# Performance work log

Hardware: AMD Instinct MI355X
Metric: run time of the kernel (lower is better)

## Reference

```python
import jax, jax.numpy as jnp
import numpy as np

B, T, C, HS = 4, 2048, 1024, 64

def setup_inputs() -> dict:
    key = jax.random.key(0)
    k1, k2, k3, k4 = jax.random.split(key, 4)
    # weights stored as [n_embd, head_size] so projection is x @ W
    scale = C ** -0.5
    return {
        "x": jax.random.normal(k1, (B, T, C), dtype=jnp.float32),
        "Wq": jax.random.normal(k2, (C, HS), dtype=jnp.float32) * scale,
        "Wk": jax.random.normal(k3, (C, HS), dtype=jnp.float32) * scale,
        "Wv": jax.random.normal(k4, (C, HS), dtype=jnp.float32) * scale,
    }

def reference(x, Wq, Wk, Wv):
    # single-head causal attention: softmax(QK^T / sqrt(hs)) V, dropout p=0 (eval)
    q = x @ Wq  # [B,T,hs]
    k = x @ Wk
    v = x @ Wv
    hs = k.shape[-1]
    wei = jnp.einsum('bqh,bkh->bqk', q, k) * (hs ** -0.5)  # [B,T,T]
    causal = jnp.tril(jnp.ones((q.shape[1], q.shape[1]), dtype=bool))
    wei = jnp.where(causal[None, :, :], wei, -jnp.inf)
    wei = jax.nn.softmax(wei, axis=-1)
    out = jnp.einsum('bqk,bkh->bqh', wei, v)  # [B,T,hs]
    return out
```

## Files before the change

### kernel.cpp

```cpp
#include <hip/hip_runtime.h>
#include <stdint.h>

#define NB 4
#define NT 2048
#define NC 1024
#define NH 64
#define NM (NB*NT)

typedef unsigned short u16;
typedef unsigned int u32;
typedef __bf16 bf16_t;
typedef float f32x4 __attribute__((ext_vector_type(4)));
typedef bf16_t bf16x8 __attribute__((ext_vector_type(8)));
typedef u16 u16x8 __attribute__((ext_vector_type(8)));
typedef u16 u16x4 __attribute__((ext_vector_type(4)));

__device__ __forceinline__ u16 f2b(float f) {
  return __builtin_bit_cast(u16, (bf16_t)f);
}

__device__ __forceinline__ void gl16(const void* g, void* l) {
  __builtin_amdgcn_global_load_lds(
      (const __attribute__((address_space(1))) u32*)g,
      (__attribute__((address_space(3))) u32*)l, 16, 0, 0);
}

__global__ __launch_bounds__(256) void wt_kernel(const float* __restrict__ Wq,
                                                 const float* __restrict__ Wk,
                                                 const float* __restrict__ Wv,
                                                 u16* __restrict__ wt) {
  __shared__ float t[64][65];
  const int m = blockIdx.x >> 4;
  const int kt = blockIdx.x & 15;
  const int k0 = kt * 64;
  const float* W = (m == 0) ? Wq : (m == 1) ? Wk : Wv;
  {
    const int r = threadIdx.x >> 2, c4 = threadIdx.x & 3;
    #pragma unroll
    for (int j = 0; j < 4; ++j) {
      const float4 f = *(const float4*)(W + (size_t)(k0 + r) * NH + c4 * 16 + j * 4);
      t[r][c4 * 16 + j * 4 + 0] = f.x;
      t[r][c4 * 16 + j * 4 + 1] = f.y;
      t[r][c4 * 16 + j * 4 + 2] = f.z;
      t[r][c4 * 16 + j * 4 + 3] = f.w;
    }
  }
  __syncthreads();
  const int n = threadIdx.x >> 2, kc = threadIdx.x & 3;
  u16x8 a, b;
  #pragma unroll
  for (int j = 0; j < 8; ++j) a[j] = f2b(t[kc * 16 + j][n]);
  #pragma unroll
  for (int j = 0; j < 8; ++j) b[j] = f2b(t[kc * 16 + 8 + j][n]);
  u16* dst = wt + ((size_t)(m * 64 + n)) * NC + k0 + kc * 16;
  *(u16x8*)dst = a;
  *(u16x8*)(dst + 8) = b;
}

__global__ __launch_bounds__(256, 2) void proj_kernel(const float* __restrict__ x,
                                                      const u16* __restrict__ wt,
                                                      u16* __restrict__ qo,
                                                      u16* __restrict__ ko,
                                                      u16* __restrict__ vto) {
  __shared__ float fA[2][16 * 64];
  __shared__ u16 sB[2][192 * 64];
  const int tid = threadIdx.x;
  const int lane = tid & 63;
  const int w = tid >> 6;
  const int g = lane >> 4;
  const int li = lane & 15;
  const int row0 = blockIdx.x * 16;
  const int wbase = tid & 0xC0;

  const f32x4 zero = {0.f, 0.f, 0.f, 0.f};
  f32x4 acc[3];
  #pragma unroll
  for (int i = 0; i < 3; ++i) acc[i] = zero;

  const int ar = tid >> 4;
  const int ac = tid & 15;
  const float* asrc0 = x + (size_t)(row0 + ar) * NC + ((ac ^ (ar & 7)) * 4);

  auto stage = [&](int kt, int nxt) {
    const int k0 = kt * 64;
    gl16(asrc0 + k0, (char*)fA[nxt] + wbase * 16);
    #pragma unroll
    for (int j = 0; j < 6; ++j) {
      const int cid = j * 256 + tid;
      const int n = cid >> 3, c = cid & 7;
      gl16(wt + (size_t)n * NC + k0 + ((c ^ (n & 7)) * 8),
           (char*)sB[nxt] + (j * 256 + wbase) * 16);
    }
  };

  stage(0, 0);
  __syncthreads();

  for (int kt = 0; kt < 16; ++kt) {
    const int cur = kt & 1;
    if (kt < 15) stage(kt + 1, cur ^ 1);
    #pragma unroll
    for (int ks = 0; ks < 2; ++ks) {
      const int c0 = ks * 8 + g * 2;
      const f32x4 a0 = *(const f32x4*)&fA[cur][li * 64 + ((c0 ^ (li & 7)) * 4)];
      const f32x4 a1 = *(const f32x4*)&fA[cur][li * 64 + (((c0 + 1) ^ (li & 7)) * 4)];
      bf16x8 a;
      a[0]=(bf16_t)a0.x; a[1]=(bf16_t)a0.y; a[2]=(bf16_t)a0.z; a[3]=(bf16_t)a0.w;
      a[4]=(bf16_t)a1.x; a[5]=(bf16_t)a1.y; a[6]=(bf16_t)a1.z; a[7]=(bf16_t)a1.w;
      #pragma unroll
      for (int f = 0; f < 3; ++f) {
        const int n = (w * 3 + f) * 16 + li;
        const bf16x8 b = *(const bf16x8*)&sB[cur][n * 64 + (((ks * 4 + g) ^ (n & 7)) * 8)];
        acc[f] = __builtin_amdgcn_mfma_f32_16x16x32_bf16(a, b, acc[f], 0, 0, 0);
      }
    }
    __syncthreads();
  }

  const int rr0 = row0 + g * 4;
  #pragma unroll
  for (int f = 0; f < 3; ++f) {
    const int fn = w * 3 + f;
    if (fn < 4) {
      #pragma unroll
      for (int i = 0; i < 4; ++i)
        qo[(size_t)(rr0 + i) * NH + fn * 16 + li] = f2b(acc[f][i]);
    } else if (fn < 8) {
      #pragma unroll
      for (int i = 0; i < 4; ++i)
        ko[(size_t)(rr0 + i) * NH + (fn - 4) * 16 + li] = f2b(acc[f][i]);
    } else {
      u16x4 pv;
      #pragma unroll
      for (int i = 0; i < 4; ++i) pv[i] = f2b(acc[f][i]);
      const int hs = (fn - 8) * 16 + li;
      const int bidx = rr0 >> 11;
      const int tt = rr0 & 2047;
      const int tile = tt >> 6, off = tt & 63;
      *(u16x4*)&vto[(((size_t)(bidx * 32 + tile) * 64) + hs) * 64 + off] = pv;
    }
  }
}

struct AttnGrp {
  union {
    u16 K[2][32 * 64];
    struct { float mo[2][16][64]; float ml[2][16]; } mg;
  } u;
};

__global__ __launch_bounds__(512) void attn_kernel(const u16* __restrict__ qg,
                                                   const u16* __restrict__ kg,
                                                   const u16* __restrict__ vtg,
                                                   float* __restrict__ out) {
  __shared__ AttnGrp grp[8];
  __shared__ u16 sP[8][16 * 32];
  const int tid = threadIdx.x;
  const int lane = tid & 63;
  const int s = tid >> 6;
  const int g = lane >> 4;
  const int li = lane & 15;
  const int jA = blockIdx.x & 63;
  const int bb = blockIdx.x >> 6;
  const int jB = 127 - jA;
  const size_t bt0 = (size_t)bb * NT;
  const int q0A = jA * 16, q0B = jB * 16;
  const int n1 = (jA >> 1) + 1;
  const int nB = 64 - (jA >> 1);

  bf16x8 aqA[2], aqB[2];
  #pragma unroll
  for (int ks = 0; ks < 2; ++ks) {
    aqA[ks] = *(const bf16x8*)(qg + (bt0 + q0A + li) * NH + ks * 32 + g * 8);
    aqB[ks] = *(const bf16x8*)(qg + (bt0 + q0B + li) * NH + ks * 32 + g * 8);
  }

  const f32x4 zero = {0.f, 0.f, 0.f, 0.f};
  f32x4 oA[4], oB[4];
  float lA[4], lB[4];
  #pragma unroll
  for (int i = 0; i < 4; ++i) { oA[i] = zero; oB[i] = zero; lA[i] = 0.f; lB[i] = 0.f; }

  auto stageK = [&](int t, int b) {
    const size_t kbase = bt0 + (size_t)t * 32;
    #pragma unroll
    for (int jj = 0; jj < 4; ++jj) {
      const int idx = jj * 64 + lane;
      const int n = idx >> 3, c = idx & 7;
      gl16(kg + (kbase + n) * NH + ((c ^ (n & 7)) * 8),
           (char*)grp[s].u.K[b] + jj * 1024);
    }
  };

  auto computeT = [&](const bf16x8 (&aq)[2], f32x4 (&o)[4], float (&ls)[4],
                      int q0, int kv0, int b, const bf16x8 (&vf)[4]) {
    f32x4 sc2[2] = {zero, zero};
    #pragma unroll
    for (int ks = 0; ks < 2; ++ks) {
      #pragma unroll
      for (int fn = 0; fn < 2; ++fn) {
        const int n = fn * 16 + li;
        const bf16x8 bk = *(const bf16x8*)&grp[s].u.K[b][n * 64 + (((ks * 4 + g) ^ (n & 7)) * 8)];
        sc2[fn] = __builtin_amdgcn_mfma_f32_16x16x32_bf16(aq[ks], bk, sc2[fn], 0, 0, 0);
      }
    }
    const bool needmask = (kv0 + 31 > q0);
    #pragma unroll
    for (int fn = 0; fn < 2; ++fn) {
      #pragma unroll
      for (int i = 0; i < 4; ++i) {
        const int q = g * 4 + i;
        float v = sc2[fn][i] * 0.125f;
        if (needmask && (kv0 + fn * 16 + li > q0 + q)) v = -1e30f;
        const float e = __expf(v);
        ls[i] += e;
        const int kc = fn * 2 + (li >> 3);
        sP[s][q * 32 + ((kc ^ (q & 3) ^ ((q >> 2) & 3)) * 8) + (li & 7)] = f2b(e);
      }
    }
    const bf16x8 pa = *(const bf16x8*)&sP[s][li * 32 + ((g ^ (li & 3) ^ ((li >> 2) & 3)) * 8)];
    #pragma unroll
    for (int fn = 0; fn < 4; ++fn)
      o[fn] = __builtin_amdgcn_mfma_f32_16x16x32_bf16(pa, vf[fn], o[fn], 0, 0, 0);
  };

  stageK(s, 0);
  int k = 0;
  for (int t = s; t < nB; t += 8, ++k) {
    bf16x8 vf[4];
    const size_t vrow = ((size_t)(bb * 32 + (t >> 1))) * 64;
    const int hoff = (t & 1) * 32;
    #pragma unroll
    for (int fn = 0; fn < 4; ++fn)
      vf[fn] = *(const bf16x8*)(vtg + (vrow + fn * 16 + li) * 64 + hoff + g * 8);

    if (t + 8 < nB) {
      stageK(t + 8, (k + 1) & 1);
      asm volatile("s_waitcnt vmcnt(8)" ::: "memory");
    } else {
      asm volatile("s_waitcnt vmcnt(4)" ::: "memory");
    }
    const int b = k & 1;
    computeT(aqB, oB, lB, q0B, t * 32, b, vf);
    if (t < n1) computeT(aqA, oA, lA, q0A, t * 32, b, vf);
  }

  #pragma unroll
  for (int i = 0; i < 4; ++i) {
    float a = lA[i], c = lB[i];
    a += __shfl_xor(a, 1); c += __shfl_xor(c, 1);
    a += __shfl_xor(a, 2); c += __shfl_xor(c, 2);
    a += __shfl_xor(a, 4); c += __shfl_xor(c, 4);
    a += __shfl_xor(a, 8); c += __shfl_xor(c, 8);
    lA[i] = a; lB[i] = c;
  }

  #pragma unroll
  for (int fn = 0; fn < 4; ++fn) {
    #pragma unroll
    for (int i = 0; i < 4; ++i) {
      grp[s].u.mg.mo[0][g * 4 + i][fn * 16 + li] = oA[fn][i];
      grp[s].u.mg.mo[1][g * 4 + i][fn * 16 + li] = oB[fn][i];
    }
  }
  if (li == 0) {
    #pragma unroll
    for (int i = 0; i < 4; ++i) {
      grp[s].u.mg.ml[0][g * 4 + i] = lA[i];
      grp[s].u.mg.ml[1][g * 4 + i] = lB[i];
    }
  }
  __syncthreads();

  {
    const int base = tid * 4;
    const int tile = base >> 10;
    const int r = (base >> 6) & 15;
    const int c0 = base & 63;
    float L = 0.f;
    f32x4 acc = zero;
    #pragma unroll
    for (int s8 = 0; s8 < 8; ++s8) {
      L += grp[s8].u.mg.ml[tile][r];
      acc += *(const f32x4*)&grp[s8].u.mg.mo[tile][r][c0];
    }
    const int row = (tile ? q0B : q0A) + r;
    const float inv = 1.f / L;
    acc *= inv;
    *(f32x4*)&out[(bt0 + row) * NH + c0] = acc;
  }
}

extern "C" void kernel_launch(void* const* d_in, const int* in_sizes, int n_in,
                              void* d_out, int out_size, void* d_ws, size_t ws_size,
                              hipStream_t stream) {
  (void)in_sizes; (void)n_in; (void)out_size; (void)ws_size;
  const float* x  = (const float*)d_in[0];
  const float* Wq = (const float*)d_in[1];
  const float* Wk = (const float*)d_in[2];
  const float* Wv = (const float*)d_in[3];
  float* out = (float*)d_out;
  char* ws = (char*)d_ws;
  u16* qb  = (u16*)(ws);
  u16* kb  = (u16*)(ws + (1u << 20));
  u16* vtb = (u16*)(ws + (2u << 20));
  u16* wtb = (u16*)(ws + (3u << 20));
  hipLaunchKernelGGL(wt_kernel,   dim3(48),  dim3(256), 0, stream, Wq, Wk, Wv, wtb);
  hipLaunchKernelGGL(proj_kernel, dim3(512), dim3(256), 0, stream, x, wtb, qb, kb, vtb);
  hipLaunchKernelGGL(attn_kernel, dim3(256), dim3(512), 0, stream, qb, kb, vtb, out);
}
```

Baseline: 38.55 us.

## Retile QKV projection to 64-row split-K blocks with separate merge kernel

The projection kernel now computes 64 rows per block over a quarter of the K dimension, reusing each B fragment across four row tiles. It drops the old double-buffered 16-row pipeline for two single-buffered 128-wide stages. Partial sums are written as bf16 to a workspace, and a new merge kernel adds the four splits and scatters them into the Q, K and transposed-V layouts. This cuts weight reloads from LDS per output row, but adds an extra launch, extra global traffic for the partials, bf16 rounding of those partials, and less load/compute overlap.

```diff
diff --git a/kernel.cpp b/kernel.cpp
--- a/kernel.cpp
+++ b/kernel.cpp
@@ -17,6 +17,9 @@
 
 __device__ __forceinline__ u16 f2b(float f) {
   return __builtin_bit_cast(u16, (bf16_t)f);
+}
+__device__ __forceinline__ float b2f(u16 u) {
+  return (float)__builtin_bit_cast(bf16_t, u);
 }
 
 __device__ __forceinline__ void gl16(const void* g, void* l) {
@@ -57,88 +60,117 @@
   *(u16x8*)(dst + 8) = b;
 }
 
-__global__ __launch_bounds__(256, 2) void proj_kernel(const float* __restrict__ x,
-                                                      const u16* __restrict__ wt,
-                                                      u16* __restrict__ qo,
-                                                      u16* __restrict__ ko,
-                                                      u16* __restrict__ vto) {
-  __shared__ float fA[2][16 * 64];
-  __shared__ u16 sB[2][192 * 64];
+__global__ __launch_bounds__(256) void proj_kernel(const float* __restrict__ x,
+                                                   const u16* __restrict__ wt,
+                                                   u16* __restrict__ pc) {
+  __shared__ float sA[64 * 128];
+  __shared__ u16 sB[192 * 128];
   const int tid = threadIdx.x;
   const int lane = tid & 63;
-  const int w = tid >> 6;
+  const int cg = tid >> 6;
   const int g = lane >> 4;
   const int li = lane & 15;
-  const int row0 = blockIdx.x * 16;
+  const int msel = blockIdx.x >> 2;
+  const int split = blockIdx.x & 3;
+  const int row0 = msel * 64;
   const int wbase = tid & 0xC0;
 
   const f32x4 zero = {0.f, 0.f, 0.f, 0.f};
-  f32x4 acc[3];
-  #pragma unroll
-  for (int i = 0; i < 3; ++i) acc[i] = zero;
-
-  const int ar = tid >> 4;
-  const int ac = tid & 15;
-  const float* asrc0 = x + (size_t)(row0 + ar) * NC + ((ac ^ (ar & 7)) * 4);
-
-  auto stage = [&](int kt, int nxt) {
-    const int k0 = kt * 64;
-    gl16(asrc0 + k0, (char*)fA[nxt] + wbase * 16);
-    #pragma unroll
-    for (int j = 0; j < 6; ++j) {
-      const int cid = j * 256 + tid;
-      const int n = cid >> 3, c = cid & 7;
-      gl16(wt + (size_t)n * NC + k0 + ((c ^ (n & 7)) * 8),
-           (char*)sB[nxt] + (j * 256 + wbase) * 16);
+  f32x4 acc[4][3];
+  #pragma unroll
+  for (int rt = 0; rt < 4; ++rt)
+    #pragma unroll
+    for (int f = 0; f < 3; ++f) acc[rt][f] = zero;
+
+  auto stage = [&](int h) {
+    const int kf = split * 256 + h * 128;
+    #pragma unroll
+    for (int j = 0; j < 8; ++j) {
+      const int slot = j * 256 + tid;
+      const int r = slot >> 5, c = slot & 31;
+      gl16(x + (size_t)(row0 + r) * NC + kf + ((c ^ (r & 7)) * 4),
+           (char*)sA + (j * 256 + wbase) * 16);
+    }
+    #pragma unroll
+    for (int j = 0; j < 12; ++j) {
+      const int slot = j * 256 + tid;
+      const int n = slot >> 4, c = slot & 15;
+      gl16(wt + (size_t)n * NC + kf + ((c ^ (n & 7)) * 8),
+           (char*)sB + (j * 256 + wbase) * 16);
     }
   };
 
-  stage(0, 0);
-  __syncthreads();
-
-  for (int kt = 0; kt < 16; ++kt) {
-    const int cur = kt & 1;
-    if (kt < 15) stage(kt + 1, cur ^ 1);
-    #pragma unroll
-    for (int ks = 0; ks < 2; ++ks) {
-      const int c0 = ks * 8 + g * 2;
-      const f32x4 a0 = *(const f32x4*)&fA[cur][li * 64 + ((c0 ^ (li & 7)) * 4)];
-      const f32x4 a1 = *(const f32x4*)&fA[cur][li * 64 + (((c0 + 1) ^ (li & 7)) * 4)];
-      bf16x8 a;
-      a[0]=(bf16_t)a0.x; a[1]=(bf16_t)a0.y; a[2]=(bf16_t)a0.z; a[3]=(bf16_t)a0.w;
-      a[4]=(bf16_t)a1.x; a[5]=(bf16_t)a1.y; a[6]=(bf16_t)a1.z; a[7]=(bf16_t)a1.w;
+  #pragma unroll
+  for (int h = 0; h < 2; ++h) {
+    stage(h);
+    asm volatile("s_waitcnt vmcnt(0)" ::: "memory");
+    __syncthreads();
+    #pragma unroll
+    for (int s = 0; s < 4; ++s) {
+      bf16x8 aF[4];
+      #pragma unroll
+      for (int rt = 0; rt < 4; ++rt) {
+        const int r = rt * 16 + li;
+        const int c0 = s * 8 + g * 2;
+        const f32x4 a0 = *(const f32x4*)&sA[r * 128 + ((c0 ^ (r & 7)) * 4)];
+        const f32x4 a1 = *(const f32x4*)&sA[r * 128 + (((c0 + 1) ^ (r & 7)) * 4)];
+        bf16x8 v;
+        v[0]=(bf16_t)a0.x; v[1]=(bf16_t)a0.y; v[2]=(bf16_t)a0.z; v[3]=(bf16_t)a0.w;
+        v[4]=(bf16_t)a1.x; v[5]=(bf16_t)a1.y; v[6]=(bf16_t)a1.z; v[7]=(bf16_t)a1.w;
+        aF[rt] = v;
+      }
       #pragma unroll
       for (int f = 0; f < 3; ++f) {
-        const int n = (w * 3 + f) * 16 + li;
-        const bf16x8 b = *(const bf16x8*)&sB[cur][n * 64 + (((ks * 4 + g) ^ (n & 7)) * 8)];
-        acc[f] = __builtin_amdgcn_mfma_f32_16x16x32_bf16(a, b, acc[f], 0, 0, 0);
+        const int n = (cg * 3 + f) * 16 + li;
+        const bf16x8 bF = *(const bf16x8*)&sB[n * 128 + (((s * 4 + g) ^ (n & 7)) * 8)];
+        #pragma unroll
+        for (int rt = 0; rt < 4; ++rt)
+          acc[rt][f] = __builtin_amdgcn_mfma_f32_16x16x32_bf16(aF[rt], bF, acc[rt][f], 0, 0, 0);
       }
     }
-    __syncthreads();
-  }
-
-  const int rr0 = row0 + g * 4;
-  #pragma unroll
-  for (int f = 0; f < 3; ++f) {
-    const int fn = w * 3 + f;
-    if (fn < 4) {
+    if (h == 0) __syncthreads();
+  }
+
+  #pragma unroll
+  for (int rt = 0; rt < 4; ++rt) {
+    const int rr0 = row0 + rt * 16 + g * 4;
+    #pragma unroll
+    for (int f = 0; f < 3; ++f) {
+      const int col = (cg * 3 + f) * 16 + li;
       #pragma unroll
       for (int i = 0; i < 4; ++i)
-        qo[(size_t)(rr0 + i) * NH + fn * 16 + li] = f2b(acc[f][i]);
-    } else if (fn < 8) {
-      #pragma unroll
-      for (int i = 0; i < 4; ++i)
-        ko[(size_t)(rr0 + i) * NH + (fn - 4) * 16 + li] = f2b(acc[f][i]);
-    } else {
-      u16x4 pv;
-      #pragma unroll
-      for (int i = 0; i < 4; ++i) pv[i] = f2b(acc[f][i]);
-      const int hs = (fn - 8) * 16 + li;
-      const int bidx = rr0 >> 11;
-      const int tt = rr0 & 2047;
-      const int tile = tt >> 6, off = tt & 63;
-      *(u16x4*)&vto[(((size_t)(bidx * 32 + tile) * 64) + hs) * 64 + off] = pv;
-    }
+        pc[((size_t)split * NM + rr0 + i) * 192 + col] = f2b(acc[rt][f][i]);
+    }
+  }
+}
+
+__global__ __launch_bounds__(256) void pmerge_kernel(const u16* __restrict__ pc,
+                                                     u16* __restrict__ qo,
+                                                     u16* __restrict__ ko,
+                                                     u16* __restrict__ vto) {
+  const int gid = blockIdx.x * 256 + threadIdx.x;
+  const int row = gid / 48;
+  const int c0 = (gid % 48) * 4;
+  float s0 = 0.f, s1 = 0.f, s2 = 0.f, s3 = 0.f;
+  #pragma unroll
+  for (int s = 0; s < 4; ++s) {
+    const u16x4 v = *(const u16x4*)&pc[((size_t)s * NM + row) * 192 + c0];
+    s0 += b2f(v[0]); s1 += b2f(v[1]); s2 += b2f(v[2]); s3 += b2f(v[3]);
+  }
+  u16x4 o;
+  o[0] = f2b(s0); o[1] = f2b(s1); o[2] = f2b(s2); o[3] = f2b(s3);
+  if (c0 < 64) {
+    *(u16x4*)&qo[(size_t)row * NH + c0] = o;
+  } else if (c0 < 128) {
+    *(u16x4*)&ko[(size_t)row * NH + (c0 - 64)] = o;
+  } else {
+    const int hs0 = c0 - 128;
+    const int bidx = row >> 11;
+    const int tt = row & 2047;
+    const int tile = tt >> 6, off = tt & 63;
+    #pragma unroll
+    for (int i = 0; i < 4; ++i)
+      vto[(((size_t)(bidx * 32 + tile) * 64) + hs0 + i) * 64 + off] = o[i];
   }
 }
 
@@ -305,7 +337,9 @@
   u16* kb  = (u16*)(ws + (1u << 20));
   u16* vtb = (u16*)(ws + (2u << 20));
   u16* wtb = (u16*)(ws + (3u << 20));
-  hipLaunchKernelGGL(wt_kernel,   dim3(48),  dim3(256), 0, stream, Wq, Wk, Wv, wtb);
-  hipLaunchKernelGGL(proj_kernel, dim3(512), dim3(256), 0, stream, x, wtb, qb, kb, vtb);
-  hipLaunchKernelGGL(attn_kernel, dim3(256), dim3(512), 0, stream, qb, kb, vtb, out);
-}
+  u16* pcb = (u16*)(ws + (3u << 20) + (512u << 10));
+  hipLaunchKernelGGL(wt_kernel,     dim3(48),   dim3(256), 0, stream, Wq, Wk, Wv, wtb);
+  hipLaunchKernelGGL(proj_kernel,   dim3(512),  dim3(256), 0, stream, x, wtb, pcb);
+  hipLaunchKernelGGL(pmerge_kernel, dim3(1536), dim3(256), 0, stream, pcb, qb, kb, vtb);
+  hipLaunchKernelGGL(attn_kernel,   dim3(256),  dim3(512), 0, stream, qb, kb, vtb, out);
+}
```

After: 44.12 us. 1.14x slower.
